# Kernel tuning notes

Hardware: AMD Instinct MI355X
Metric: run time of the kernel (lower is better)

## Reference

```python
import jax, jax.numpy as jnp
import numpy as np

N_TREES = 10
N_DEPTH = 8
IN_DIM = 2048
CLASSES = 1000
BATCH = 16384
N_DECISION = 2 ** N_DEPTH - 1          # 255
N_LEAF = 2 ** (N_DEPTH + 1)            # 512 (module's own convention)


def _tiling_pattern():
    # Static gather pattern mapping each (leaf, depth) slot to an index into
    # the packed [decision_p, 1 - decision_p] tensor, exactly as in the source.
    tp = np.zeros((N_LEAF, N_DEPTH), dtype=np.int32)
    dec_idx = 0
    for n in range(N_DEPTH):
        j = 0
        for _ in range(2 ** n):
            rep = 2 ** (N_DEPTH - n)
            tp[j:j + rep, n] = dec_idx
            j += rep
            tp[j:j + rep, n] = N_DECISION + dec_idx
            j += rep
            dec_idx += 1
    return tp.reshape(-1)

FLAT_PATTERN = jnp.asarray(_tiling_pattern())  # [N_LEAF * N_DEPTH]


def setup_inputs() -> dict:
    key = jax.random.key(0)
    kx, kd, kl = jax.random.split(key, 3)
    x = jax.random.normal(kx, (BATCH, IN_DIM), dtype=jnp.float32)
    # small scale so sigmoid logits are not fully saturated (mimics uniform init)
    w_d = jax.random.normal(kd, (N_TREES, IN_DIM, N_DECISION), dtype=jnp.float32) * 0.02
    w_l = jax.random.normal(kl, (N_TREES, N_LEAF, CLASSES), dtype=jnp.float32)
    return {"x": x, "w_d": w_d, "w_l": w_l}


def reference(x, w_d, w_l):
    # decision probabilities for all trees: [T, B, N_DECISION]
    decision_p = jax.nn.sigmoid(jnp.einsum('bi,tid->tbd', x, w_d))
    # packed [p, 1-p]: [T, B, 2*N_DECISION]
    pack = jnp.concatenate([decision_p, 1.0 - decision_p], axis=-1)
    # static gather -> path probability factors: [T, B, N_LEAF, N_DEPTH]
    mu = pack[..., FLAT_PATTERN].reshape(N_TREES, x.shape[0], N_LEAF, N_DEPTH)
    leaf_prob = jnp.prod(mu, axis=-1)               # [T, B, N_LEAF]
    leaf_p = jax.nn.softmax(w_l, axis=-1)           # [T, N_LEAF, C]
    # sum over trees, then average
    return jnp.einsum('tbl,tlc->bc', leaf_prob, leaf_p) / N_TREES
```

## Files before the change

kernel.cpp:

```cpp
#include <hip/hip_runtime.h>
#include <stdint.h>

#define T_TREES 10
#define IN_DIM  2048
#define BATCH   16384
#define CLASSES 1000
#define NDEC    255
#define NPAD    256
#define K2DIM   (T_TREES * NPAD)
#define NPADC   1024

typedef unsigned short u16;
typedef float floatx4 __attribute__((ext_vector_type(4)));
typedef __bf16 bf16x8 __attribute__((ext_vector_type(8)));

__device__ __forceinline__ u16 f2bf(float f) {
    union { float f; uint32_t u; } v; v.f = f;
    uint32_t u = v.u;
    return (u16)((u + 0x7FFFu + ((u >> 16) & 1u)) >> 16);
}
__device__ __forceinline__ float bf2f(u16 h) {
    union { uint32_t u; float f; } v; v.u = ((uint32_t)h) << 16;
    return v.f;
}

__device__ __forceinline__ void gld16(u16* lds_p, const u16* g) {
    __builtin_amdgcn_global_load_lds(
        (__attribute__((address_space(1))) const void*)g,
        (__attribute__((address_space(3))) void*)lds_p,
        16, 0, 0);
}

__global__ __launch_bounds__(256) void cast_x_k(const float4* __restrict__ x,
                                                uint2* __restrict__ xb) {
    int i = blockIdx.x * 256 + threadIdx.x;
    float4 v = x[i];
    uint2 o;
    o.x = (uint32_t)f2bf(v.x) | ((uint32_t)f2bf(v.y) << 16);
    o.y = (uint32_t)f2bf(v.z) | ((uint32_t)f2bf(v.w) << 16);
    xb[i] = o;
}

__global__ void transpose_wd_k(const float* __restrict__ wd, u16* __restrict__ wdT) {
    __shared__ float tile[32][33];
    int tx = threadIdx.x, ty = threadIdx.y;
    int t = blockIdx.z;
    int i0 = blockIdx.x * 32, d0 = blockIdx.y * 32;
#pragma unroll
    for (int r = 0; r < 4; ++r) {
        int i = i0 + ty + r * 8;
        int d = d0 + tx;
        float v = (d < NDEC) ? wd[((size_t)t * IN_DIM + i) * NDEC + d] : 0.0f;
        tile[ty + r * 8][tx] = v;
    }
    __syncthreads();
#pragma unroll
    for (int r = 0; r < 4; ++r) {
        int dd = d0 + ty + r * 8;
        int ii = i0 + tx;
        wdT[((size_t)t * NPAD + dd) * IN_DIM + ii] = f2bf(tile[tx][ty + r * 8]);
    }
}

__global__ __launch_bounds__(256) void softmax_fold_k(const float* __restrict__ wl,
                                                      u16* __restrict__ B2) {
    int wid = threadIdx.x >> 6, lane = threadIdx.x & 63;
    int idx = blockIdx.x * 4 + wid;
    int t = idx >> 8, m = idx & 255;
    const float* r0 = wl + ((size_t)t * 512 + 2 * m) * CLASSES;
    const float* r1 = r0 + CLASSES;
    float v0[16], v1[16];
    float mx0 = -3.0e38f, mx1 = -3.0e38f;
#pragma unroll
    for (int j = 0; j < 16; ++j) {
        int c = lane + 64 * j;
        float a = (c < CLASSES) ? r0[c] : -3.0e38f;
        float b = (c < CLASSES) ? r1[c] : -3.0e38f;
        v0[j] = a; v1[j] = b;
        mx0 = fmaxf(mx0, a); mx1 = fmaxf(mx1, b);
    }
#pragma unroll
    for (int o = 32; o > 0; o >>= 1) {
        mx0 = fmaxf(mx0, __shfl_xor(mx0, o));
        mx1 = fmaxf(mx1, __shfl_xor(mx1, o));
    }
    float s0 = 0.f, s1 = 0.f;
#pragma unroll
    for (int j = 0; j < 16; ++j) {
        int c = lane + 64 * j;
        float e0 = (c < CLASSES) ? __expf(v0[j] - mx0) : 0.f;
        float e1 = (c < CLASSES) ? __expf(v1[j] - mx1) : 0.f;
        v0[j] = e0; v1[j] = e1; s0 += e0; s1 += e1;
    }
#pragma unroll
    for (int o = 32; o > 0; o >>= 1) { s0 += __shfl_xor(s0, o); s1 += __shfl_xor(s1, o); }
    float i0 = 0.1f / s0, i1 = 0.1f / s1;
#pragma unroll
    for (int j = 0; j < 16; ++j) {
        int c = lane + 64 * j;
        float v = (c < CLASSES) ? (v0[j] * i0 + v1[j] * i1) : 0.f;
        B2[(size_t)idx * NPADC + c] = f2bf(v);
    }
}

__global__ void transpose_b2_k(const u16* __restrict__ B2, u16* __restrict__ B2t) {
    __shared__ u16 tile[32][33];
    int tx = threadIdx.x, ty = threadIdx.y;
    int k0 = blockIdx.x * 32, c0 = blockIdx.y * 32;
#pragma unroll
    for (int r = 0; r < 4; ++r)
        tile[ty + r * 8][tx] = B2[(size_t)(k0 + ty + r * 8) * NPADC + c0 + tx];
    __syncthreads();
#pragma unroll
    for (int r = 0; r < 4; ++r)
        B2t[(size_t)(c0 + ty + r * 8) * K2DIM + k0 + tx] = tile[tx][ty + r * 8];
}


#define WAITLGKM_(n) asm volatile("s_waitcnt lgkmcnt(" #n ")" ::: "memory")
#define WAITLGKM(n) WAITLGKM_(n)
#define WAITVM_(n) asm volatile("s_waitcnt vmcnt(" #n ")" ::: "memory")
#define WAITVM(n) WAITVM_(n)
#define SB  __builtin_amdgcn_sched_barrier(0)
#define BAR __builtin_amdgcn_s_barrier()

template<int NT, int EPI>
__global__ __launch_bounds__(512, 2) void gemm8p(const u16* __restrict__ A,
                                                 const u16* __restrict__ B,
                                                 void* __restrict__ Cout) {
    constexpr int K = NT * 64;
    __shared__ __align__(16) u16 lds[8 * 8192];

    const int tid  = threadIdx.x;
    const int wid  = tid >> 6;
    const int lane = tid & 63;
    const int wm = wid >> 2, wn = wid & 3;
    const int quad = lane >> 4, t16 = lane & 15;

    const size_t m0 = (size_t)blockIdx.x * 256;
    const size_t n0 = (size_t)blockIdx.y * 256;
    const u16* __restrict__ Ag = A + m0 * (size_t)K;
    const u16* __restrict__ Bg = B + n0 * (size_t)K;

    const uint32_t stOff = (uint32_t)((wid * 8 + (lane >> 3)) * K)
                         + (uint32_t)(((lane & 7) ^ ((lane >> 3) & 7)) * 8);
    const uint32_t stLds = (uint32_t)(wid * 8 * 64);

#define STAGE(slot, o, tk) do { \
    const u16* gp_ = (((o) < 2) ? Bg : Ag) + ((size_t)(((o) & 1) * 128) * K) \
                   + ((size_t)(tk) * 64) + stOff; \
    gld16(&lds[(slot) * 8192 + stLds], gp_); \
    gld16(&lds[(slot) * 8192 + stLds + 4096], gp_ + (size_t)64 * K); \
  } while (0)

#define AOFF(P, mi, kk) (((P) * 4 + 2 + wm) * 8192 + ((mi) * 16 + t16) * 64 \
                         + ((((kk) * 4 + quad) ^ (t16 & 7)) * 8))
#define BOFF(P, ni, kk) (((P) * 4 + (wn >> 1)) * 8192 \
                         + ((wn & 1) * 64 + (ni) * 16 + t16) * 64 \
                         + ((((kk) * 4 + quad) ^ (t16 & 7)) * 8))

#define RDA(P, mb, kk) do { \
    aF[0] = *(const bf16x8*)&lds[AOFF(P, (mb) + 0, kk)]; \
    aF[1] = *(const bf16x8*)&lds[AOFF(P, (mb) + 1, kk)]; \
    aF[2] = *(const bf16x8*)&lds[AOFF(P, (mb) + 2, kk)]; \
    aF[3] = *(const bf16x8*)&lds[AOFF(P, (mb) + 3, kk)]; \
  } while (0)

#define RDBF(P, kk) do { \
    bF[0] = *(const bf16x8*)&lds[BOFF(P, 0, kk)]; \
    bF[1] = *(const bf16x8*)&lds[BOFF(P, 1, kk)]; \
    bF[2] = *(const bf16x8*)&lds[BOFF(P, 2, kk)]; \
    bF[3] = *(const bf16x8*)&lds[BOFF(P, 3, kk)]; \
  } while (0)

#define MF16(mb) do { \
    _Pragma("unroll") \
    for (int ni_ = 0; ni_ < 4; ++ni_) { \
      _Pragma("unroll") \
      for (int j_ = 0; j_ < 4; ++j_) { \
        acc[(mb) + j_][ni_] = __builtin_amdgcn_mfma_f32_16x16x32_bf16( \
            aF[j_], bF[ni_], acc[(mb) + j_][ni_], 0, 0, 0); \
      } \
    } \
  } while (0)

    floatx4 acc[8][4];
#pragma unroll
    for (int i = 0; i < 8; ++i)
#pragma unroll
        for (int j = 0; j < 4; ++j) acc[i][j] = (floatx4){0.f, 0.f, 0.f, 0.f};

    bf16x8 aF[4], bF[4];

    STAGE(0, 0, 0); STAGE(1, 1, 0); STAGE(2, 2, 0); STAGE(3, 3, 0);
    STAGE(4, 0, 1); STAGE(5, 1, 1);
    WAITVM(4);
    BAR;

#define TILE(P, t, SA, SBG, HASW, WN) do { \
     \
    RDA(P, 0, 0); RDBF(P, 0); \
    if (SA) { STAGE((1 - (P)) * 4 + 2, 2, (t) + 1); \
              STAGE((1 - (P)) * 4 + 3, 3, (t) + 1); } \
    BAR; WAITLGKM(0); SB; \
    __builtin_amdgcn_s_setprio(1); MF16(0); __builtin_amdgcn_s_setprio(0); \
    BAR; \
     \
    RDA(P, 4, 0); \
    BAR; WAITLGKM(0); SB; \
    __builtin_amdgcn_s_setprio(1); MF16(4); __builtin_amdgcn_s_setprio(0); \
    BAR; \
     \
    RDA(P, 0, 1); RDBF(P, 1); \
    BAR; WAITLGKM(0); SB; \
    __builtin_amdgcn_s_setprio(1); MF16(0); __builtin_amdgcn_s_setprio(0); \
    BAR; \
     \
    RDA(P, 4, 1); \
    if (SBG) { STAGE((P) * 4 + 0, 0, (t) + 2); \
               STAGE((P) * 4 + 1, 1, (t) + 2); } \
    if (HASW) { WAITVM(WN); } \
    BAR; WAITLGKM(0); SB; \
    __builtin_amdgcn_s_setprio(1); MF16(4); __builtin_amdgcn_s_setprio(0); \
    BAR; \
  } while (0)

    int t = 0;
#pragma unroll 1
    for (int it = 0; it < NT / 2 - 1; ++it, t += 2) {
        TILE(0, t,     true, true, true, 4);
        TILE(1, t + 1, true, true, true, 4);
    }
    TILE(0, NT - 2, true,  false, true,  0);
    TILE(1, NT - 1, false, false, false, 0);

    if constexpr (EPI == 0) {
        u16* C = (u16*)Cout;
#pragma unroll
        for (int mi = 0; mi < 8; ++mi)
#pragma unroll
            for (int r = 0; r < 4; ++r) {
                const size_t row = m0 + wm * 128 + mi * 16 + quad * 4 + r;
#pragma unroll
                for (int ni = 0; ni < 4; ++ni) {
                    const int col = (int)n0 + wn * 64 + ni * 16 + t16;
                    float v = acc[mi][ni][r];
                    float p = 1.0f / (1.0f + __expf(-v));
                    C[row * (size_t)K2DIM + col] = f2bf(p);
                }
            }
    } else {
        float* C = (float*)Cout;
#pragma unroll
        for (int mi = 0; mi < 8; ++mi)
#pragma unroll
            for (int r = 0; r < 4; ++r) {
                const size_t row = m0 + wm * 128 + mi * 16 + quad * 4 + r;
#pragma unroll
                for (int ni = 0; ni < 4; ++ni) {
                    const int col = (int)n0 + wn * 64 + ni * 16 + t16;
                    if (col < CLASSES)
                        C[row * (size_t)CLASSES + col] = acc[mi][ni][r];
                }
            }
    }
#undef TILE
#undef MF16
#undef RDBF
#undef RDA
#undef BOFF
#undef AOFF
#undef STAGE
}

__global__ __launch_bounds__(256) void leafprod_k(const u16* __restrict__ dp,
                                                  u16* __restrict__ lp) {
    __shared__ float P[4][256];
    int wid = threadIdx.x >> 6, lane = threadIdx.x & 63;
    int idx = blockIdx.x * 4 + wid;
    int t = idx >> 14, b = idx & 16383;
    const u16* row = dp + (size_t)b * K2DIM + t * NPAD;
#pragma unroll
    for (int j = 0; j < 4; ++j)
        P[wid][lane + 64 * j] = bf2f(row[lane + 64 * j]);
    __syncthreads();
#pragma unroll
    for (int j = 0; j < 4; ++j) {
        int m = lane + 64 * j;
        float prod = 1.0f;
#pragma unroll
        for (int n = 0; n < 8; ++n) {
            int dec  = (1 << n) - 1 + (m >> (8 - n));
            int side = (m >> (7 - n)) & 1;
            float p  = P[wid][dec];
            prod *= side ? (1.0f - p) : p;
        }
        lp[(size_t)b * K2DIM + t * NPAD + m] = f2bf(prod);
    }
}

extern "C" void kernel_launch(void* const* d_in, const int* in_sizes, int n_in,
                              void* d_out, int out_size, void* d_ws, size_t ws_size,
                              hipStream_t stream) {
    const float* x   = (const float*)d_in[0];
    const float* w_d = (const float*)d_in[1];
    const float* w_l = (const float*)d_in[2];
    float* out = (float*)d_out;

    char* w = (char*)d_ws;
    u16* B2t = (u16*)w;
    char* region = w + 5242880;
    u16* xb  = (u16*)region;
    u16* wdT = (u16*)(region + 67108864);
    u16* B2  = (u16*)(region + 67108864 + 10485760);
    u16* lp  = (u16*)region;
    u16* dp  = (u16*)(region + 83886080);

    cast_x_k<<<32768, 256, 0, stream>>>((const float4*)x, (uint2*)xb);
    transpose_wd_k<<<dim3(64, 8, T_TREES), dim3(32, 8), 0, stream>>>(w_d, wdT);
    softmax_fold_k<<<640, 256, 0, stream>>>(w_l, B2);
    transpose_b2_k<<<dim3(80, 32), dim3(32, 8), 0, stream>>>(B2, B2t);
    gemm8p<32, 0><<<dim3(64, 10), 512, 0, stream>>>(xb, wdT, dp);
    leafprod_k<<<40960, 256, 0, stream>>>(dp, lp);
    gemm8p<40, 1><<<dim3(64, 4), 512, 0, stream>>>(lp, B2t, out);
}
```

Measured before the change: 522.5 us.

## Fuse leaf-product into decision GEMM epilogue and retile GEMM to 128x256

Rewrites the bf16 GEMM kernel to use 128-row by 256-column tiles with a K-step of 32, smaller LDS, and a launch bound allowing 4 blocks per CU. In the first GEMM, the sigmoid outputs for one tree are written to swizzled LDS, and each wave then computes the path-probability products for 16 rows and writes leaf probabilities directly. This removes the separate leafprod kernel and the round trip of the decision-probability tensor through global memory, and raises occupancy. The trade-off is a shorter K step, which means more barriers per unit of work, plus a smaller M tile, which means less reuse of the B operand.

```diff
diff --git a/kernel.cpp b/kernel.cpp
--- a/kernel.cpp
+++ b/kernel.cpp
@@ -125,11 +125,11 @@
 #define BAR __builtin_amdgcn_s_barrier()
 
 template<int NT, int EPI>
-__global__ __launch_bounds__(512, 2) void gemm8p(const u16* __restrict__ A,
-                                                 const u16* __restrict__ B,
-                                                 void* __restrict__ Cout) {
-    constexpr int K = NT * 64;
-    __shared__ __align__(16) u16 lds[8 * 8192];
+__global__ __launch_bounds__(512, 4) void gemmF(const u16* __restrict__ A,
+                                                const u16* __restrict__ B,
+                                                void* __restrict__ Cout) {
+    constexpr int K = NT * 32;
+    __shared__ __align__(16) u16 lds[(EPI == 0) ? 32768 : 24576];
 
     const int tid  = threadIdx.x;
     const int wid  = tid >> 6;
@@ -137,125 +137,128 @@
     const int wm = wid >> 2, wn = wid & 3;
     const int quad = lane >> 4, t16 = lane & 15;
 
-    const size_t m0 = (size_t)blockIdx.x * 256;
-    const size_t n0 = (size_t)blockIdx.y * 256;
+    const size_t m0 = (size_t)blockIdx.x * 128;
     const u16* __restrict__ Ag = A + m0 * (size_t)K;
-    const u16* __restrict__ Bg = B + n0 * (size_t)K;
-
-    const uint32_t stOff = (uint32_t)((wid * 8 + (lane >> 3)) * K)
-                         + (uint32_t)(((lane & 7) ^ ((lane >> 3) & 7)) * 8);
-    const uint32_t stLds = (uint32_t)(wid * 8 * 64);
-
-#define STAGE(slot, o, tk) do { \
-    const u16* gp_ = (((o) < 2) ? Bg : Ag) + ((size_t)(((o) & 1) * 128) * K) \
-                   + ((size_t)(tk) * 64) + stOff; \
-    gld16(&lds[(slot) * 8192 + stLds], gp_); \
-    gld16(&lds[(slot) * 8192 + stLds + 4096], gp_ + (size_t)64 * K); \
+    const u16* __restrict__ Bg = B + (size_t)blockIdx.y * 256 * (size_t)K;
+
+    const uint32_t stRow = (uint32_t)(wid * 16 + (lane >> 2));
+    const uint32_t stSeg = (uint32_t)((lane & 3) * 8);
+    const u16* pa  = Ag + (size_t)stRow * K + stSeg;
+    const u16* pb0 = Bg + (size_t)stRow * K + stSeg;
+    const u16* pb1 = pb0 + (size_t)128 * K;
+    u16* const ldsA = &lds[wid * 512];
+    u16* const ldsB = &lds[8192 + wid * 512];
+
+#define STAGEA(par, koff) gld16(ldsA + (par) * 4096, pa + (koff))
+#define STAGEB(par, koff) do { \
+    gld16(ldsB + (par) * 8192,        pb0 + (koff)); \
+    gld16(ldsB + (par) * 8192 + 4096, pb1 + (koff)); \
   } while (0)
 
-#define AOFF(P, mi, kk) (((P) * 4 + 2 + wm) * 8192 + ((mi) * 16 + t16) * 64 \
-                         + ((((kk) * 4 + quad) ^ (t16 & 7)) * 8))
-#define BOFF(P, ni, kk) (((P) * 4 + (wn >> 1)) * 8192 \
-                         + ((wn & 1) * 64 + (ni) * 16 + t16) * 64 \
-                         + ((((kk) * 4 + quad) ^ (t16 & 7)) * 8))
-
-#define RDA(P, mb, kk) do { \
-    aF[0] = *(const bf16x8*)&lds[AOFF(P, (mb) + 0, kk)]; \
-    aF[1] = *(const bf16x8*)&lds[AOFF(P, (mb) + 1, kk)]; \
-    aF[2] = *(const bf16x8*)&lds[AOFF(P, (mb) + 2, kk)]; \
-    aF[3] = *(const bf16x8*)&lds[AOFF(P, (mb) + 3, kk)]; \
-  } while (0)
-
-#define RDBF(P, kk) do { \
-    bF[0] = *(const bf16x8*)&lds[BOFF(P, 0, kk)]; \
-    bF[1] = *(const bf16x8*)&lds[BOFF(P, 1, kk)]; \
-    bF[2] = *(const bf16x8*)&lds[BOFF(P, 2, kk)]; \
-    bF[3] = *(const bf16x8*)&lds[BOFF(P, 3, kk)]; \
-  } while (0)
-
-#define MF16(mb) do { \
+#define AOFF(P, mi) ((P) * 4096 + (wm * 64 + (mi) * 16 + t16) * 32 + quad * 8)
+#define BOFF(P, ni) (8192 + (P) * 8192 + (wn * 64 + (ni) * 16 + t16) * 32 + quad * 8)
+
+#define MF8(mb, a0_, a1_) do { \
     _Pragma("unroll") \
     for (int ni_ = 0; ni_ < 4; ++ni_) { \
-      _Pragma("unroll") \
-      for (int j_ = 0; j_ < 4; ++j_) { \
-        acc[(mb) + j_][ni_] = __builtin_amdgcn_mfma_f32_16x16x32_bf16( \
-            aF[j_], bF[ni_], acc[(mb) + j_][ni_], 0, 0, 0); \
-      } \
+      acc[(mb)][ni_]     = __builtin_amdgcn_mfma_f32_16x16x32_bf16( \
+          a0_, bF[ni_], acc[(mb)][ni_], 0, 0, 0); \
+      acc[(mb) + 1][ni_] = __builtin_amdgcn_mfma_f32_16x16x32_bf16( \
+          a1_, bF[ni_], acc[(mb) + 1][ni_], 0, 0, 0); \
     } \
   } while (0)
 
-    floatx4 acc[8][4];
-#pragma unroll
-    for (int i = 0; i < 8; ++i)
+    floatx4 acc[4][4];
+#pragma unroll
+    for (int i = 0; i < 4; ++i)
 #pragma unroll
         for (int j = 0; j < 4; ++j) acc[i][j] = (floatx4){0.f, 0.f, 0.f, 0.f};
 
-    bf16x8 aF[4], bF[4];
-
-    STAGE(0, 0, 0); STAGE(1, 1, 0); STAGE(2, 2, 0); STAGE(3, 3, 0);
-    STAGE(4, 0, 1); STAGE(5, 1, 1);
-    WAITVM(4);
+    bf16x8 aF0, aF1, aF2, aF3, bF[4];
+
+    STAGEA(0, 0);
+    STAGEB(0, 0);
+    STAGEB(1, 32);
+    WAITVM(2);
     BAR;
 
 #define TILE(P, t, SA, SBG, HASW, WN) do { \
-     \
-    RDA(P, 0, 0); RDBF(P, 0); \
-    if (SA) { STAGE((1 - (P)) * 4 + 2, 2, (t) + 1); \
-              STAGE((1 - (P)) * 4 + 3, 3, (t) + 1); } \
+    aF0   = *(const bf16x8*)&lds[AOFF(P, 0)]; \
+    aF1   = *(const bf16x8*)&lds[AOFF(P, 1)]; \
+    bF[0] = *(const bf16x8*)&lds[BOFF(P, 0)]; \
+    bF[1] = *(const bf16x8*)&lds[BOFF(P, 1)]; \
+    bF[2] = *(const bf16x8*)&lds[BOFF(P, 2)]; \
+    bF[3] = *(const bf16x8*)&lds[BOFF(P, 3)]; \
+    if (SA) { STAGEA(1 - (P), ((t) + 1) * 32); } \
     BAR; WAITLGKM(0); SB; \
-    __builtin_amdgcn_s_setprio(1); MF16(0); __builtin_amdgcn_s_setprio(0); \
+    __builtin_amdgcn_s_setprio(1); MF8(0, aF0, aF1); __builtin_amdgcn_s_setprio(0); \
     BAR; \
-     \
-    RDA(P, 4, 0); \
-    BAR; WAITLGKM(0); SB; \
-    __builtin_amdgcn_s_setprio(1); MF16(4); __builtin_amdgcn_s_setprio(0); \
-    BAR; \
-     \
-    RDA(P, 0, 1); RDBF(P, 1); \
-    BAR; WAITLGKM(0); SB; \
-    __builtin_amdgcn_s_setprio(1); MF16(0); __builtin_amdgcn_s_setprio(0); \
-    BAR; \
-     \
-    RDA(P, 4, 1); \
-    if (SBG) { STAGE((P) * 4 + 0, 0, (t) + 2); \
-               STAGE((P) * 4 + 1, 1, (t) + 2); } \
+    aF2 = *(const bf16x8*)&lds[AOFF(P, 2)]; \
+    aF3 = *(const bf16x8*)&lds[AOFF(P, 3)]; \
+    if (SBG) { STAGEB(P, ((t) + 2) * 32); } \
     if (HASW) { WAITVM(WN); } \
     BAR; WAITLGKM(0); SB; \
-    __builtin_amdgcn_s_setprio(1); MF16(4); __builtin_amdgcn_s_setprio(0); \
+    __builtin_amdgcn_s_setprio(1); MF8(2, aF2, aF3); __builtin_amdgcn_s_setprio(0); \
     BAR; \
   } while (0)
 
     int t = 0;
 #pragma unroll 1
     for (int it = 0; it < NT / 2 - 1; ++it, t += 2) {
-        TILE(0, t,     true, true, true, 4);
-        TILE(1, t + 1, true, true, true, 4);
+        TILE(0, t,     true, true, true, 2);
+        TILE(1, t + 1, true, true, true, 2);
     }
     TILE(0, NT - 2, true,  false, true,  0);
     TILE(1, NT - 1, false, false, false, 0);
 
     if constexpr (EPI == 0) {
-        u16* C = (u16*)Cout;
-#pragma unroll
-        for (int mi = 0; mi < 8; ++mi)
+#pragma unroll
+        for (int mi = 0; mi < 4; ++mi)
 #pragma unroll
             for (int r = 0; r < 4; ++r) {
-                const size_t row = m0 + wm * 128 + mi * 16 + quad * 4 + r;
+                const int rl = wm * 64 + mi * 16 + quad * 4 + r;
+                const int sw = ((rl >> 2) & 3) << 4;
 #pragma unroll
                 for (int ni = 0; ni < 4; ++ni) {
-                    const int col = (int)n0 + wn * 64 + ni * 16 + t16;
+                    const int col = wn * 64 + ni * 16 + t16;
                     float v = acc[mi][ni][r];
                     float p = 1.0f / (1.0f + __expf(-v));
-                    C[row * (size_t)K2DIM + col] = f2bf(p);
+                    lds[rl * 256 + (col ^ sw)] = f2bf(p);
                 }
             }
+        BAR;
+        u16* LP = (u16*)Cout;
+#pragma unroll 1
+        for (int rr = 0; rr < 16; ++rr) {
+            const int rl = wid * 16 + rr;
+            const int csw = ((rl >> 2) & 3) << 4;
+            const u16* Prow = &lds[rl * 256];
+            float pre = 1.0f;
+#pragma unroll
+            for (int n = 0; n < 6; ++n) {
+                const int dec  = (1 << n) - 1 + (lane >> (6 - n));
+                const int side = (lane >> (5 - n)) & 1;
+                const float p = bf2f(Prow[dec ^ csw]);
+                pre *= side ? (1.0f - p) : p;
+            }
+            const float p6 = bf2f(Prow[(63 + lane) ^ csw]);
+            const float e0 = pre * p6, e1 = pre * (1.0f - p6);
+            const float pA = bf2f(Prow[(127 + 2 * lane) ^ csw]);
+            const float pB = bf2f(Prow[(127 + 2 * lane + 1) ^ csw]);
+            ushort4 o;
+            o.x = f2bf(e0 * pA); o.y = f2bf(e0 * (1.0f - pA));
+            o.z = f2bf(e1 * pB); o.w = f2bf(e1 * (1.0f - pB));
+            const size_t row = m0 + rl;
+            *(ushort4*)&LP[row * K2DIM + (size_t)blockIdx.y * 256 + 4 * lane] = o;
+        }
     } else {
         float* C = (float*)Cout;
-#pragma unroll
-        for (int mi = 0; mi < 8; ++mi)
+        const size_t n0 = (size_t)blockIdx.y * 256;
+#pragma unroll
+        for (int mi = 0; mi < 4; ++mi)
 #pragma unroll
             for (int r = 0; r < 4; ++r) {
-                const size_t row = m0 + wm * 128 + mi * 16 + quad * 4 + r;
+                const size_t row = m0 + wm * 64 + mi * 16 + quad * 4 + r;
 #pragma unroll
                 for (int ni = 0; ni < 4; ++ni) {
                     const int col = (int)n0 + wn * 64 + ni * 16 + t16;
@@ -265,38 +268,11 @@
             }
     }
 #undef TILE
-#undef MF16
-#undef RDBF
-#undef RDA
+#undef MF8
 #undef BOFF
 #undef AOFF
-#undef STAGE
-}
-
-__global__ __launch_bounds__(256) void leafprod_k(const u16* __restrict__ dp,
-                                                  u16* __restrict__ lp) {
-    __shared__ float P[4][256];
-    int wid = threadIdx.x >> 6, lane = threadIdx.x & 63;
-    int idx = blockIdx.x * 4 + wid;
-    int t = idx >> 14, b = idx & 16383;
-    const u16* row = dp + (size_t)b * K2DIM + t * NPAD;
-#pragma unroll
-    for (int j = 0; j < 4; ++j)
-        P[wid][lane + 64 * j] = bf2f(row[lane + 64 * j]);
-    __syncthreads();
-#pragma unroll
-    for (int j = 0; j < 4; ++j) {
-        int m = lane + 64 * j;
-        float prod = 1.0f;
-#pragma unroll
-        for (int n = 0; n < 8; ++n) {
-            int dec  = (1 << n) - 1 + (m >> (8 - n));
-            int side = (m >> (7 - n)) & 1;
-            float p  = P[wid][dec];
-            prod *= side ? (1.0f - p) : p;
-        }
-        lp[(size_t)b * K2DIM + t * NPAD + m] = f2bf(prod);
-    }
+#undef STAGEB
+#undef STAGEA
 }
 
 extern "C" void kernel_launch(void* const* d_in, const int* in_sizes, int n_in,
@@ -309,18 +285,15 @@
 
     char* w = (char*)d_ws;
     u16* B2t = (u16*)w;
-    char* region = w + 5242880;
-    u16* xb  = (u16*)region;
-    u16* wdT = (u16*)(region + 67108864);
-    u16* B2  = (u16*)(region + 67108864 + 10485760);
-    u16* lp  = (u16*)region;
-    u16* dp  = (u16*)(region + 83886080);
+    u16* xb  = (u16*)(w + 5242880);
+    u16* wdT = (u16*)(w + 5242880 + 67108864);
+    u16* B2  = (u16*)(w + 5242880 + 67108864 + 10485760);
+    u16* lp  = (u16*)(w + 5242880 + 67108864 + 10485760 + 5242880);
 
     cast_x_k<<<32768, 256, 0, stream>>>((const float4*)x, (uint2*)xb);
     transpose_wd_k<<<dim3(64, 8, T_TREES), dim3(32, 8), 0, stream>>>(w_d, wdT);
     softmax_fold_k<<<640, 256, 0, stream>>>(w_l, B2);
     transpose_b2_k<<<dim3(80, 32), dim3(32, 8), 0, stream>>>(B2, B2t);
-    gemm8p<32, 0><<<dim3(64, 10), 512, 0, stream>>>(xb, wdT, dp);
-    leafprod_k<<<40960, 256, 0, stream>>>(dp, lp);
-    gemm8p<40, 1><<<dim3(64, 4), 512, 0, stream>>>(lp, B2t, out);
-}
+    gemmF<64, 0><<<dim3(128, T_TREES), 512, 0, stream>>>(xb, wdT, lp);
+    gemmF<80, 1><<<dim3(128, 4), 512, 0, stream>>>(lp, B2t, out);
+}
```

After: 515.9 us. No clear change (-1.3%).
